# Performance work log

Measured on AMD Instinct MI355X. Metric: run time of the kernel, lower is better.

The kernel has to match this reference:

```python
import jax, jax.numpy as jnp
import numpy as np

MARGIN = 0.3
EPS = 1e-12

def setup_inputs() -> dict:
    key = jax.random.key(0)
    k1, k2 = jax.random.split(key)
    n, d, num_classes = 8192, 512, 512
    inputs = jax.random.normal(k1, (n, d), dtype=jnp.float32)
    targets = jax.random.randint(k2, (n,), 0, num_classes, dtype=jnp.int64)
    return {"inputs": inputs, "targets": targets}

def reference(inputs, targets):
    n = inputs.shape[0]
    # pairwise Euclidean distances: ||xi||^2 + ||xj||^2 - 2 xi.xj, clamped & sqrt'd
    sq = jnp.sum(inputs * inputs, axis=1)  # [n]
    dist2 = sq[:, None] + sq[None, :] - 2.0 * (inputs @ inputs.T)
    dist = jnp.sqrt(jnp.clip(dist2, EPS, None))  # [n, n]
    mask = targets[:, None] == targets[None, :]  # [n, n] same-identity mask
    neg_inf = jnp.asarray(-jnp.inf, dist.dtype)
    pos_inf = jnp.asarray(jnp.inf, dist.dtype)
    dist_ap = jnp.max(jnp.where(mask, dist, neg_inf), axis=1)   # hardest positive per row
    dist_an = jnp.min(jnp.where(mask, pos_inf, dist), axis=1)   # hardest negative per row
    # MarginRankingLoss with y=1, mean reduction: mean(relu(dist_ap - dist_an + margin))
    loss = jnp.mean(jnp.maximum(dist_ap - dist_an + MARGIN, 0.0))
    return loss
```

## Files before the change

### kernel.cpp

```cpp
#include <hip/hip_runtime.h>

#define N 8192
#define D 512
#define NOFF 496
#define NDIAG 32
#define NBRICKS (NOFF + NDIAG)
#define MARGIN 0.3f

typedef __attribute__((ext_vector_type(4))) int int4v;
typedef __attribute__((ext_vector_type(8))) int int8v;
typedef __attribute__((ext_vector_type(4))) float f32x4;

__device__ __forceinline__ void gload_lds16(const void* g, void* l) {
    __builtin_amdgcn_global_load_lds(
        (const __attribute__((address_space(1))) void*)g,
        (__attribute__((address_space(3))) void*)l,
        16, 0, 0);
}

__device__ __forceinline__ int8v load_frag8(const unsigned char* base, int row, int q) {
    const int v = (2 * q) ^ (row & 7);
    int4v lo = *(const int4v*)(base + row * 128 + v * 16);
    int4v hi = *(const int4v*)(base + row * 128 + (v ^ 1) * 16);
    return __builtin_shufflevector(lo, hi, 0, 1, 2, 3, 4, 5, 6, 7);
}

__device__ __forceinline__ void stage_tile(const unsigned char* Ag, unsigned char* Asm,
                                           const unsigned char* Bg, unsigned char* Bsm,
                                           int tid, int k0) {
    #pragma unroll
    for (int s = 0; s < 4; s++) {
        int p = s * 512 + tid;
        int r = p >> 3, kc = (p & 7) ^ (r & 7);
        gload_lds16(Ag + (size_t)r * D + k0 + kc * 16, Asm + p * 16);
    }
    #pragma unroll
    for (int s = 0; s < 4; s++) {
        int p = s * 512 + tid;
        int r = p >> 3, kc = (p & 7) ^ (r & 7);
        gload_lds16(Bg + (size_t)r * D + k0 + kc * 16, Bsm + p * 16);
    }
}

__global__ void prep_kernel(const float* __restrict__ x,
                            unsigned char* __restrict__ x8,
                            float* __restrict__ sq,
                            unsigned int* __restrict__ apU,
                            unsigned int* __restrict__ anU,
                            int* __restrict__ cnt) {
    if (blockIdx.x == 0 && threadIdx.x == 0) cnt[0] = 0;
    int w = threadIdx.x >> 6, lane = threadIdx.x & 63;
    int row = blockIdx.x * 4 + w;
    const float4* p = (const float4*)(x + (size_t)row * D) + lane * 2;
    float4 v0 = p[0], v1 = p[1];
    float s = v0.x * v0.x + v0.y * v0.y + v0.z * v0.z + v0.w * v0.w
            + v1.x * v1.x + v1.y * v1.y + v1.z * v1.z + v1.w * v1.w;
    int w0 = __builtin_amdgcn_cvt_pk_fp8_f32(v0.x, v0.y, 0, false);
    w0     = __builtin_amdgcn_cvt_pk_fp8_f32(v0.z, v0.w, w0, true);
    int w1 = __builtin_amdgcn_cvt_pk_fp8_f32(v1.x, v1.y, 0, false);
    w1     = __builtin_amdgcn_cvt_pk_fp8_f32(v1.z, v1.w, w1, true);
    ((int2*)(x8 + (size_t)row * D))[lane] = make_int2(w0, w1);
    #pragma unroll
    for (int o = 32; o > 0; o >>= 1) s += __shfl_xor(s, o);
    if (lane == 0) {
        sq[row] = s;
        apU[row] = 0u;
        anU[row] = 0x7f800000u;
    }
}

__global__ __launch_bounds__(512, 2)
void gemm_kernel(const unsigned char* __restrict__ xb,
                 const float* __restrict__ sq,
                 const int* __restrict__ tgt,
                 unsigned int* __restrict__ apU,
                 unsigned int* __restrict__ anU) {
    __shared__ __align__(16) char smem_raw[65536];
    __shared__ float sqI[256], sqJ[256];
    __shared__ int tI[256], tJ[256];

    unsigned char* Asm = (unsigned char*)smem_raw;
    unsigned char* Bsm = Asm + 32768;
    float* rowPap = (float*)smem_raw;
    float* rowPan = rowPap + 256;
    float* colPap = rowPan + 256;
    float* colPan = colPap + 256 * 5;

    const int id = (blockIdx.x & 7) * 66 + (blockIdx.x >> 3);
    int ri, cj;
    if (id < NOFF) {
        cj = (int)((1.0f + sqrtf(1.0f + 8.0f * (float)id)) * 0.5f);
        while (cj * (cj - 1) / 2 > id) cj--;
        while ((cj + 1) * cj / 2 <= id) cj++;
        ri = id - cj * (cj - 1) / 2;
    } else {
        ri = cj = id - NOFF;
    }
    const int rowBase = ri * 256, colBase = cj * 256;

    const int tid = threadIdx.x;
    const int w = tid >> 6, lane = tid & 63, q = lane >> 4, c = lane & 15;
    const int wm = w & 3, wn = w >> 2;

    if (tid < 256) {
        sqI[tid] = sq[rowBase + tid]; tI[tid] = tgt[rowBase + tid];
        sqJ[tid] = sq[colBase + tid]; tJ[tid] = tgt[colBase + tid];
    }

    const unsigned char* Ag = xb + (size_t)rowBase * D;
    const unsigned char* Bg = xb + (size_t)colBase * D;

    f32x4 acc[4][8] = {};

    stage_tile(Ag, Asm, Bg, Bsm, tid, 0);

    #pragma unroll
    for (int kk = 0; kk < 4; kk++) {
        __syncthreads();
        int8v af[4], b0[4];
        #pragma unroll
        for (int t = 0; t < 4; t++)
            af[t] = load_frag8(Asm, wm * 64 + t * 16 + c, q);
        #pragma unroll
        for (int t = 0; t < 4; t++)
            b0[t] = load_frag8(Bsm, wn * 128 + t * 16 + c, q);
        #pragma unroll
        for (int tm = 0; tm < 4; tm++)
            #pragma unroll
            for (int t = 0; t < 4; t++)
                acc[tm][t] = __builtin_amdgcn_mfma_scale_f32_16x16x128_f8f6f4(
                    af[tm], b0[t], acc[tm][t],
                    0, 0,
                    0, 0x7F7F7F7Fu, 0, 0x7F7F7F7Fu);
        int8v b1[4];
        #pragma unroll
        for (int t = 0; t < 4; t++)
            b1[t] = load_frag8(Bsm, wn * 128 + (4 + t) * 16 + c, q);
        __syncthreads();
        if (kk < 3)
            stage_tile(Ag, Asm, Bg, Bsm, tid, (kk + 1) * 128);
        #pragma unroll
        for (int tm = 0; tm < 4; tm++)
            #pragma unroll
            for (int t = 0; t < 4; t++)
                acc[tm][4 + t] = __builtin_amdgcn_mfma_scale_f32_16x16x128_f8f6f4(
                    af[tm], b1[t], acc[tm][4 + t],
                    0, 0, 0, 0x7F7F7F7Fu, 0, 0x7F7F7F7Fu);
    }

    float sjc[8]; int tjx[8];
    #pragma unroll
    for (int tn = 0; tn < 8; tn++) {
        int col_l = wn * 128 + tn * 16 + c;
        sjc[tn] = sqJ[col_l]; tjx[tn] = tJ[col_l];
    }
    float apc[8], anc[8];
    #pragma unroll
    for (int tn = 0; tn < 8; tn++) { apc[tn] = -1e30f; anc[tn] = 1e30f; }
    float rpk[4][4], rnk[4][4];
    #pragma unroll
    for (int tm = 0; tm < 4; tm++) {
        #pragma unroll
        for (int r = 0; r < 4; r++) {
            int row_l = wm * 64 + tm * 16 + q * 4 + r;
            float si = sqI[row_l]; int ti = tI[row_l];
            float rp = -1e30f, rn = 1e30f;
            #pragma unroll
            for (int tn = 0; tn < 8; tn++) {
                float p = acc[tm][tn][r];
                bool same = (ti == tjx[tn]);
                float rk = fmaf(-2.0f, p, sjc[tn]);
                float ck = fmaf(-2.0f, p, si);
                rp = fmaxf(rp, same ? rk : -1e30f);
                rn = fminf(rn, same ? 1e30f : rk);
                apc[tn] = fmaxf(apc[tn], same ? ck : -1e30f);
                anc[tn] = fminf(anc[tn], same ? 1e30f : ck);
            }
            #pragma unroll
            for (int o = 1; o < 16; o <<= 1) {
                rp = fmaxf(rp, __shfl_xor(rp, o));
                rn = fminf(rn, __shfl_xor(rn, o));
            }
            rpk[tm][r] = rp; rnk[tm][r] = rn;
        }
    }
    if (wn == 1 && c == 0) {
        #pragma unroll
        for (int tm = 0; tm < 4; tm++)
            #pragma unroll
            for (int r = 0; r < 4; r++) {
                int row_l = wm * 64 + tm * 16 + q * 4 + r;
                rowPap[row_l] = rpk[tm][r];
                rowPan[row_l] = rnk[tm][r];
            }
    }
    #pragma unroll
    for (int tn = 0; tn < 8; tn++) {
        apc[tn] = fmaxf(apc[tn], __shfl_xor(apc[tn], 16));
        apc[tn] = fmaxf(apc[tn], __shfl_xor(apc[tn], 32));
        anc[tn] = fminf(anc[tn], __shfl_xor(anc[tn], 16));
        anc[tn] = fminf(anc[tn], __shfl_xor(anc[tn], 32));
    }
    if (q == 0) {
        #pragma unroll
        for (int tn = 0; tn < 8; tn++) {
            int col_l = wn * 128 + tn * 16 + c;
            colPap[col_l * 5 + wm] = apc[tn];
            colPan[col_l * 5 + wm] = anc[tn];
        }
    }
    __syncthreads();
    if (wn == 0 && c == 0) {
        #pragma unroll
        for (int tm = 0; tm < 4; tm++)
            #pragma unroll
            for (int r = 0; r < 4; r++) {
                int row_l = wm * 64 + tm * 16 + q * 4 + r;
                float ap = fmaxf(rpk[tm][r], rowPap[row_l]);
                float an = fminf(rnk[tm][r], rowPan[row_l]);
                float apd = fmaxf(sqI[row_l] + ap, 0.0f);
                float and_ = fmaxf(sqI[row_l] + an, 0.0f);
                atomicMax(&apU[rowBase + row_l], __float_as_uint(apd));
                atomicMin(&anU[rowBase + row_l], __float_as_uint(and_));
            }
    }
    if (tid < 256) {
        float ap = -1e30f, an = 1e30f;
        #pragma unroll
        for (int u = 0; u < 4; u++) {
            ap = fmaxf(ap, colPap[tid * 5 + u]);
            an = fminf(an, colPan[tid * 5 + u]);
        }
        float apd = fmaxf(sqJ[tid] + ap, 0.0f);
        float and_ = fmaxf(sqJ[tid] + an, 0.0f);
        atomicMax(&apU[colBase + tid], __float_as_uint(apd));
        atomicMin(&anU[colBase + tid], __float_as_uint(and_));
    }
}

__global__ void reduce_kernel(const unsigned int* __restrict__ apU,
                              const unsigned int* __restrict__ anU,
                              float* __restrict__ bsum, int* __restrict__ cnt,
                              float* __restrict__ out) {
    int tid = threadIdx.x;
    int row = blockIdx.x * 256 + tid;
    float ap = __uint_as_float(apU[row]);
    float an = __uint_as_float(anU[row]);
    float dap = sqrtf(fmaxf(ap, 1e-12f));
    float dan = sqrtf(fmaxf(an, 1e-12f));
    float v = fmaxf(dap - dan + MARGIN, 0.0f);
    #pragma unroll
    for (int o = 32; o > 0; o >>= 1) v += __shfl_xor(v, o);
    __shared__ float ss[4];
    __shared__ int amLast;
    if ((tid & 63) == 0) ss[tid >> 6] = v;
    __syncthreads();
    if (tid == 0) {
        bsum[blockIdx.x] = ss[0] + ss[1] + ss[2] + ss[3];
        __threadfence();
        amLast = (atomicAdd(cnt, 1) == N / 256 - 1);
    }
    __syncthreads();
    if (amLast && tid < 64) {
        __threadfence();
        float t = (tid < N / 256) ? bsum[tid] : 0.0f;
        #pragma unroll
        for (int o = 32; o > 0; o >>= 1) t += __shfl_xor(t, o);
        if (tid == 0) out[0] = t * (1.0f / (float)N);
    }
}

extern "C" void kernel_launch(void* const* d_in, const int* in_sizes, int n_in,
                              void* d_out, int out_size, void* d_ws, size_t ws_size,
                              hipStream_t stream) {
    const float* x  = (const float*)d_in[0];
    const int* tgt  = (const int*)d_in[1];
    float* out      = (float*)d_out;

    char* ws = (char*)d_ws;
    unsigned char* x8 = (unsigned char*)ws;
    float* sq   = (float*)(ws + (size_t)N * D);
    unsigned int* apU = (unsigned int*)(sq + N);
    unsigned int* anU = apU + N;
    float* bsum = (float*)(anU + N);
    int* cnt = (int*)(bsum + 32);

    prep_kernel<<<N / 4, 256, 0, stream>>>(x, x8, sq, apU, anU, cnt);
    gemm_kernel<<<NBRICKS, 512, 0, stream>>>(x8, sq, tgt, apU, anU);
    reduce_kernel<<<N / 256, 256, 0, stream>>>(apU, anU, bsum, cnt, out);
}
```

Before: 123.4 us.

## Shrink symmetric GEMM tiles to 128x128 with 256-thread blocks

Halves the triangular tile size from 256x256 to 128x128, so the kernel launches 2080 blocks of 256 threads instead of 528 blocks of 512, with smaller LDS buffers and a simpler two-way column reduction. The goal is better load balance across CUs and higher occupancy in exchange for more global traffic per FLOP, more tiles to stage and more atomics. The software overlap also changes, since the first MFMA half no longer runs before the barrier.

```diff
diff --git a/kernel.cpp b/kernel.cpp
--- a/kernel.cpp
+++ b/kernel.cpp
@@ -2,9 +2,9 @@
 
 #define N 8192
 #define D 512
-#define NOFF 496
-#define NDIAG 32
-#define NBRICKS (NOFF + NDIAG)
+#define NOFFD 2016
+#define NDIAG 64
+#define NBRICKS (NOFFD + NDIAG)
 #define MARGIN 0.3f
 
 typedef __attribute__((ext_vector_type(4))) int int4v;
@@ -30,13 +30,13 @@
                                            int tid, int k0) {
     #pragma unroll
     for (int s = 0; s < 4; s++) {
-        int p = s * 512 + tid;
+        int p = s * 256 + tid;
         int r = p >> 3, kc = (p & 7) ^ (r & 7);
         gload_lds16(Ag + (size_t)r * D + k0 + kc * 16, Asm + p * 16);
     }
     #pragma unroll
     for (int s = 0; s < 4; s++) {
-        int p = s * 512 + tid;
+        int p = s * 256 + tid;
         int r = p >> 3, kc = (p & 7) ^ (r & 7);
         gload_lds16(Bg + (size_t)r * D + k0 + kc * 16, Bsm + p * 16);
     }
@@ -69,40 +69,36 @@
     }
 }
 
-__global__ __launch_bounds__(512, 2)
+__global__ __launch_bounds__(256, 3)
 void gemm_kernel(const unsigned char* __restrict__ xb,
                  const float* __restrict__ sq,
                  const int* __restrict__ tgt,
                  unsigned int* __restrict__ apU,
                  unsigned int* __restrict__ anU) {
-    __shared__ __align__(16) char smem_raw[65536];
-    __shared__ float sqI[256], sqJ[256];
-    __shared__ int tI[256], tJ[256];
-
-    unsigned char* Asm = (unsigned char*)smem_raw;
-    unsigned char* Bsm = Asm + 32768;
-    float* rowPap = (float*)smem_raw;
-    float* rowPan = rowPap + 256;
-    float* colPap = rowPan + 256;
-    float* colPan = colPap + 256 * 5;
-
-    const int id = (blockIdx.x & 7) * 66 + (blockIdx.x >> 3);
+    __shared__ __align__(16) unsigned char Asm[16384];
+    __shared__ __align__(16) unsigned char Bsm[16384];
+    __shared__ float sqI[128], sqJ[128];
+    __shared__ int tI[128], tJ[128];
+    __shared__ float rowPap[128], rowPan[128];
+    __shared__ float colPap[128], colPan[128];
+
+    const int id = (blockIdx.x & 7) * 260 + (blockIdx.x >> 3);
     int ri, cj;
-    if (id < NOFF) {
+    if (id < NOFFD) {
         cj = (int)((1.0f + sqrtf(1.0f + 8.0f * (float)id)) * 0.5f);
         while (cj * (cj - 1) / 2 > id) cj--;
         while ((cj + 1) * cj / 2 <= id) cj++;
         ri = id - cj * (cj - 1) / 2;
     } else {
-        ri = cj = id - NOFF;
-    }
-    const int rowBase = ri * 256, colBase = cj * 256;
+        ri = cj = id - NOFFD;
+    }
+    const int rowBase = ri * 128, colBase = cj * 128;
 
     const int tid = threadIdx.x;
     const int w = tid >> 6, lane = tid & 63, q = lane >> 4, c = lane & 15;
-    const int wm = w & 3, wn = w >> 2;
-
-    if (tid < 256) {
+    const int wm = w & 1, wn = w >> 1;
+
+    if (tid < 128) {
         sqI[tid] = sq[rowBase + tid]; tI[tid] = tgt[rowBase + tid];
         sqJ[tid] = sq[colBase + tid]; tJ[tid] = tgt[colBase + tid];
     }
@@ -110,32 +106,20 @@
     const unsigned char* Ag = xb + (size_t)rowBase * D;
     const unsigned char* Bg = xb + (size_t)colBase * D;
 
-    f32x4 acc[4][8] = {};
+    f32x4 acc[4][4] = {};
 
     stage_tile(Ag, Asm, Bg, Bsm, tid, 0);
 
     #pragma unroll
     for (int kk = 0; kk < 4; kk++) {
         __syncthreads();
-        int8v af[4], b0[4];
+        int8v af[4], bf[4];
         #pragma unroll
         for (int t = 0; t < 4; t++)
             af[t] = load_frag8(Asm, wm * 64 + t * 16 + c, q);
         #pragma unroll
         for (int t = 0; t < 4; t++)
-            b0[t] = load_frag8(Bsm, wn * 128 + t * 16 + c, q);
-        #pragma unroll
-        for (int tm = 0; tm < 4; tm++)
-            #pragma unroll
-            for (int t = 0; t < 4; t++)
-                acc[tm][t] = __builtin_amdgcn_mfma_scale_f32_16x16x128_f8f6f4(
-                    af[tm], b0[t], acc[tm][t],
-                    0, 0,
-                    0, 0x7F7F7F7Fu, 0, 0x7F7F7F7Fu);
-        int8v b1[4];
-        #pragma unroll
-        for (int t = 0; t < 4; t++)
-            b1[t] = load_frag8(Bsm, wn * 128 + (4 + t) * 16 + c, q);
+            bf[t] = load_frag8(Bsm, wn * 64 + t * 16 + c, q);
         __syncthreads();
         if (kk < 3)
             stage_tile(Ag, Asm, Bg, Bsm, tid, (kk + 1) * 128);
@@ -143,20 +127,21 @@
         for (int tm = 0; tm < 4; tm++)
             #pragma unroll
             for (int t = 0; t < 4; t++)
-                acc[tm][4 + t] = __builtin_amdgcn_mfma_scale_f32_16x16x128_f8f6f4(
-                    af[tm], b1[t], acc[tm][4 + t],
-                    0, 0, 0, 0x7F7F7F7Fu, 0, 0x7F7F7F7Fu);
-    }
-
-    float sjc[8]; int tjx[8];
-    #pragma unroll
-    for (int tn = 0; tn < 8; tn++) {
-        int col_l = wn * 128 + tn * 16 + c;
+                acc[tm][t] = __builtin_amdgcn_mfma_scale_f32_16x16x128_f8f6f4(
+                    af[tm], bf[t], acc[tm][t],
+                    0, 0,
+                    0, 0x7F7F7F7Fu, 0, 0x7F7F7F7Fu);
+    }
+
+    float sjc[4]; int tjx[4];
+    #pragma unroll
+    for (int tn = 0; tn < 4; tn++) {
+        int col_l = wn * 64 + tn * 16 + c;
         sjc[tn] = sqJ[col_l]; tjx[tn] = tJ[col_l];
     }
-    float apc[8], anc[8];
-    #pragma unroll
-    for (int tn = 0; tn < 8; tn++) { apc[tn] = -1e30f; anc[tn] = 1e30f; }
+    float apc[4], anc[4];
+    #pragma unroll
+    for (int tn = 0; tn < 4; tn++) { apc[tn] = -1e30f; anc[tn] = 1e30f; }
     float rpk[4][4], rnk[4][4];
     #pragma unroll
     for (int tm = 0; tm < 4; tm++) {
@@ -166,7 +151,7 @@
             float si = sqI[row_l]; int ti = tI[row_l];
             float rp = -1e30f, rn = 1e30f;
             #pragma unroll
-            for (int tn = 0; tn < 8; tn++) {
+            for (int tn = 0; tn < 4; tn++) {
                 float p = acc[tm][tn][r];
                 bool same = (ti == tjx[tn]);
                 float rk = fmaf(-2.0f, p, sjc[tn]);
@@ -195,18 +180,18 @@
             }
     }
     #pragma unroll
-    for (int tn = 0; tn < 8; tn++) {
+    for (int tn = 0; tn < 4; tn++) {
         apc[tn] = fmaxf(apc[tn], __shfl_xor(apc[tn], 16));
         apc[tn] = fmaxf(apc[tn], __shfl_xor(apc[tn], 32));
         anc[tn] = fminf(anc[tn], __shfl_xor(anc[tn], 16));
         anc[tn] = fminf(anc[tn], __shfl_xor(anc[tn], 32));
     }
-    if (q == 0) {
-        #pragma unroll
-        for (int tn = 0; tn < 8; tn++) {
-            int col_l = wn * 128 + tn * 16 + c;
-            colPap[col_l * 5 + wm] = apc[tn];
-            colPan[col_l * 5 + wm] = anc[tn];
+    if (wm == 1 && q == 0) {
+        #pragma unroll
+        for (int tn = 0; tn < 4; tn++) {
+            int col_l = wn * 64 + tn * 16 + c;
+            colPap[col_l] = apc[tn];
+            colPan[col_l] = anc[tn];
         }
     }
     __syncthreads();
@@ -224,17 +209,17 @@
                 atomicMin(&anU[rowBase + row_l], __float_as_uint(and_));
             }
     }
-    if (tid < 256) {
-        float ap = -1e30f, an = 1e30f;
-        #pragma unroll
-        for (int u = 0; u < 4; u++) {
-            ap = fmaxf(ap, colPap[tid * 5 + u]);
-            an = fminf(an, colPan[tid * 5 + u]);
+    if (wm == 0 && q == 0) {
+        #pragma unroll
+        for (int tn = 0; tn < 4; tn++) {
+            int col_l = wn * 64 + tn * 16 + c;
+            float ap = fmaxf(apc[tn], colPap[col_l]);
+            float an = fminf(anc[tn], colPan[col_l]);
+            float apd = fmaxf(sqJ[col_l] + ap, 0.0f);
+            float and_ = fmaxf(sqJ[col_l] + an, 0.0f);
+            atomicMax(&apU[colBase + col_l], __float_as_uint(apd));
+            atomicMin(&anU[colBase + col_l], __float_as_uint(and_));
         }
-        float apd = fmaxf(sqJ[tid] + ap, 0.0f);
-        float and_ = fmaxf(sqJ[tid] + an, 0.0f);
-        atomicMax(&apU[colBase + tid], __float_as_uint(apd));
-        atomicMin(&anU[colBase + tid], __float_as_uint(and_));
     }
 }
 
@@ -286,6 +271,6 @@
     int* cnt = (int*)(bsum + 32);
 
     prep_kernel<<<N / 4, 256, 0, stream>>>(x, x8, sq, apU, anU, cnt);
-    gemm_kernel<<<NBRICKS, 512, 0, stream>>>(x8, sq, tgt, apU, anU);
+    gemm_kernel<<<NBRICKS, 256, 0, stream>>>(x8, sq, tgt, apU, anU);
     reduce_kernel<<<N / 256, 256, 0, stream>>>(apU, anU, bsum, cnt, out);
 }
```

Measured after the change: 112.1 us. 1.1x faster.
